# Optimization experiments

Measured on AMD Instinct MI355X. Metric: run time of the kernel, lower is better.

The kernel has to match this reference:

```python
import jax, jax.numpy as jnp
import numpy as np

VOCAB = 50257
NUM_TAGS = 50
EMB_DIM = 128
CTX = 2
N_TOKENS = 262144


def setup_inputs() -> dict:
    key = jax.random.key(0)
    k1, k2, k3, k4 = jax.random.split(key, 4)
    tokens = jax.random.randint(k1, (N_TOKENS,), 0, VOCAB, dtype=jnp.int64 if jax.config.jax_enable_x64 else jnp.int32)
    emb_table = jax.random.normal(k2, (VOCAB, EMB_DIM), dtype=jnp.float32)
    W = jax.random.normal(k3, (NUM_TAGS, EMB_DIM * (1 + 2 * CTX)), dtype=jnp.float32) * 0.05
    b = jax.random.normal(k4, (NUM_TAGS,), dtype=jnp.float32) * 0.05
    return {"tokens": tokens, "emb_table": emb_table, "W": W, "b": b}


def reference(tokens, emb_table, W, b):
    # [N, D] embedding gather
    emb = emb_table[tokens]
    n = emb.shape[0]
    # zero-pad CTX positions on each side (matches torch.zeros_like padding)
    padded = jnp.pad(emb, ((CTX, CTX), (0, 0)))
    # sliding window concat: [N, (2*CTX+1)*D] via 2*CTX+1 shifted views
    windows = jnp.concatenate([padded[i:i + n] for i in range(2 * CTX + 1)], axis=-1)
    logits = windows @ W.T + b  # [N, num_tags]
    log_probs = jax.nn.log_softmax(logits, axis=-1)
    return log_probs
```

## Files before the change

### kernel.cpp

```cpp
#include <hip/hip_runtime.h>
#include <hip/hip_bf16.h>

#define VOCAB 50257
#define NTAGS 50
#define EMB   128
#define NTOK  262144
#define KD    640
#define WPAD  64

#define TAGP  64
#define NZ    320
#define ZROWS 50304

#define TOK   24
#define RWS   28
#define CHR   40
#define NCHUNK (RWS*CHR)
#define NITER  ((NCHUNK+63)/64)

typedef __attribute__((ext_vector_type(4))) float f32x4;
typedef __attribute__((ext_vector_type(8))) short bf16x8;

__device__ __forceinline__ ushort f2bf(float f) {
    union { float f; unsigned u; } v; v.f = f;
    unsigned u = v.u;
    return (ushort)((u + 0x7fffu + ((u >> 16) & 1u)) >> 16);
}

__device__ __forceinline__ void gload_lds16(const void* g, void* l) {
    __builtin_amdgcn_global_load_lds(
        (const __attribute__((address_space(1))) unsigned*)g,
        (__attribute__((address_space(3))) unsigned*)l, 16, 0, 0);
}


__global__ void conv_k(const float* __restrict__ W, ushort* __restrict__ Wt) {
    int g = blockIdx.x * blockDim.x + threadIdx.x;
    if (g >= NZ * 16) return;
    int n = g >> 4, j = g & 15;
    int tg = n & 63, p = n >> 6;
    bf16x8 val = (bf16x8){0,0,0,0,0,0,0,0};
    if (tg < NTAGS) {
        const float* wp = W + tg * KD + p * EMB + j * 8;
        f32x4 lo = *(const f32x4*)wp;
        f32x4 hi = *(const f32x4*)(wp + 4);
        val[0]=(short)f2bf(lo[0]); val[1]=(short)f2bf(lo[1]);
        val[2]=(short)f2bf(lo[2]); val[3]=(short)f2bf(lo[3]);
        val[4]=(short)f2bf(hi[0]); val[5]=(short)f2bf(hi[1]);
        val[6]=(short)f2bf(hi[2]); val[7]=(short)f2bf(hi[3]);
    }
    *(bf16x8*)((char*)Wt + n * 256 + ((j ^ (n & 7)) << 4)) = val;
}

__global__ __launch_bounds__(256)
void zt_k(const float* __restrict__ emb, const ushort* __restrict__ Wt,
          ushort* __restrict__ ZT) {
    __shared__ __align__(16) char wlds[NZ * EMB * 2];

    const int tid  = threadIdx.x;
    const int lane = tid & 63;
    const int wave = tid >> 6;
    const int c = lane & 15, q = lane >> 4;
    const int vb = blockIdx.x * 128;

    f32x4 Elo[2][4], Ehi[2][4];
    #pragma unroll
    for (int nv = 0; nv < 2; ++nv) {
        int row = vb + wave * 32 + nv * 16 + c;
        bool ok = row < VOCAB;
        const float* rp = emb + (size_t)(ok ? row : 0) * EMB;
        #pragma unroll
        for (int kk = 0; kk < 4; ++kk) {
            Elo[nv][kk] = ok ? *(const f32x4*)(rp + kk * 32 + q * 8)
                             : (f32x4){0,0,0,0};
            Ehi[nv][kk] = ok ? *(const f32x4*)(rp + kk * 32 + q * 8 + 4)
                             : (f32x4){0,0,0,0};
        }
    }

    #pragma unroll
    for (int it = 0; it < 20; ++it) {
        int g = it * 256 + tid;
        gload_lds16((const char*)Wt + g * 16, wlds + it * 4096 + (tid >> 6) * 1024 + (tid & 63) * 16);
    }

    bf16x8 E[2][4];
    #pragma unroll
    for (int nv = 0; nv < 2; ++nv)
        #pragma unroll
        for (int kk = 0; kk < 4; ++kk) {
            bf16x8 a;
            a[0]=(short)f2bf(Elo[nv][kk][0]); a[1]=(short)f2bf(Elo[nv][kk][1]);
            a[2]=(short)f2bf(Elo[nv][kk][2]); a[3]=(short)f2bf(Elo[nv][kk][3]);
            a[4]=(short)f2bf(Ehi[nv][kk][0]); a[5]=(short)f2bf(Ehi[nv][kk][1]);
            a[6]=(short)f2bf(Ehi[nv][kk][2]); a[7]=(short)f2bf(Ehi[nv][kk][3]);
            E[nv][kk] = a;
        }
    __syncthreads();

    #pragma unroll
    for (int ng = 0; ng < 5; ++ng) {
        bf16x8 Wf[4][4];
        #pragma unroll
        for (int mtag = 0; mtag < 4; ++mtag) {
            #pragma unroll
            for (int kk = 0; kk < 4; ++kk) {
                int r  = ng * 64 + mtag * 16 + c;
                int ph = (kk * 4 + q) ^ (c & 7);
                Wf[mtag][kk] = *(const bf16x8*)(wlds + r * 256 + ph * 16);
            }
        }
        f32x4 acc[4][2];
        #pragma unroll
        for (int mtag = 0; mtag < 4; ++mtag)
            #pragma unroll
            for (int nv = 0; nv < 2; ++nv)
                acc[mtag][nv] = (f32x4){0.f,0.f,0.f,0.f};
        #pragma unroll
        for (int kk = 0; kk < 4; ++kk)
            #pragma unroll
            for (int mtag = 0; mtag < 4; ++mtag)
                #pragma unroll
                for (int nv = 0; nv < 2; ++nv)
                    acc[mtag][nv] = __builtin_amdgcn_mfma_f32_16x16x32_bf16(
                        Wf[mtag][kk], E[nv][kk], acc[mtag][nv], 0, 0, 0);
        #pragma unroll
        for (int nv = 0; nv < 2; ++nv) {
            const size_t row = (size_t)(vb + wave * 32 + nv * 16 + c);
            #pragma unroll
            for (int mtag = 0; mtag < 4; ++mtag) {
                ushort4 o = { f2bf(acc[mtag][nv][0]), f2bf(acc[mtag][nv][1]),
                              f2bf(acc[mtag][nv][2]), f2bf(acc[mtag][nv][3]) };
                *(ushort4*)(ZT + row * NZ + ng * 64 + mtag * 16 + q * 4) = o;
            }
        }
    }
}

__global__ __launch_bounds__(64, 1)
void tag_k(const int* __restrict__ tokens, const ushort* __restrict__ ZT,
           const float* __restrict__ bias, float* __restrict__ out) {
    __shared__ __align__(16) char smem[RWS * 640 + 128];
    int* ids = (int*)(smem + RWS * 640);

    const int l  = threadIdx.x;
    const int bb = blockIdx.x * TOK;

    {
        int t = bb - 2 + l;
        if (l < RWS) ids[l] = ((unsigned)t < NTOK) ? tokens[t] : VOCAB;
    }
    __syncthreads();

    int tk[NITER];
    #pragma unroll
    for (int w = 0; w < NITER; ++w) {
        int g = w * 64 + l;
        int r = (g < NCHUNK) ? (g / CHR) : 0;
        tk[w] = ids[r];
    }

    #pragma unroll
    for (int w = 0; w < NITER; ++w) {
        int g = w * 64 + l;
        if (g < NCHUNK) {
            int r  = g / CHR;
            int ch = g - r * CHR;
            int i  = ch & 7, p = ch >> 3;
            const char* src = (const char*)ZT + (size_t)tk[w] * 640
                              + p * 128 + ((i ^ (r & 7)) << 4);
            gload_lds16(src, smem + w * 1024);
        }
    }
    __syncthreads();

    float acc[56];
    #pragma unroll
    for (int g = 0; g < 12; ++g) {
        float4 b4 = *(const float4*)(bias + g * 4);
        acc[g*4+0] = b4.x; acc[g*4+1] = b4.y; acc[g*4+2] = b4.z; acc[g*4+3] = b4.w;
    }
    acc[48] = bias[48]; acc[49] = bias[49];
    #pragma unroll
    for (int j = 50; j < 56; ++j) acc[j] = 0.f;

    {
        const int le = (l < TOK) ? l : (TOK - 1);
        bf16x8 v[5][7];
        #pragma unroll
        for (int p = 0; p < 5; ++p) {
            const int rp = le + p;
            const char* rb = smem + rp * 640;
            const int rx = (rp & 7) << 4;
            #pragma unroll
            for (int j = 0; j < 7; ++j)
                v[p][j] = *(const bf16x8*)(rb + p * 128 + ((j << 4) ^ rx));
        }
        #pragma unroll
        for (int p = 0; p < 5; ++p)
            #pragma unroll
            for (int j = 0; j < 7; ++j)
                #pragma unroll
                for (int e = 0; e < 8; ++e) {
                    unsigned u = (unsigned)(ushort)v[p][j][e] << 16;
                    acc[j*8+e] += __uint_as_float(u);
                }
    }

    float m = acc[0];
    #pragma unroll
    for (int j = 1; j < NTAGS; ++j) m = fmaxf(m, acc[j]);
    float s = 0.f;
    #pragma unroll
    for (int j = 0; j < NTAGS; ++j) s += __expf(acc[j] - m);
    const float L = m + __logf(s);

    __syncthreads();
    if (l < TOK) {
        #pragma unroll
        for (int k = 0; k < 25; ++k) {
            float2 st = { acc[2*k] - L, acc[2*k+1] - L };
            *(float2*)(smem + (size_t)l * 200 + k * 8) = st;
        }
    }
    __syncthreads();
    const int nvalid = (NTOK - bb < TOK) ? (NTOK - bb) : TOK;
    const int nbytes = nvalid * 200;
    char* ob = (char*)out + (size_t)bb * 200;
    #pragma unroll
    for (int w = 0; w < 5; ++w) {
        int off = w * 1024 + l * 16;
        if (off < nbytes) {
            f32x4 d = *(const f32x4*)(smem + off);
            __builtin_nontemporal_store(d, (f32x4*)(ob + off));
        }
    }
}

__global__ void fb_conv_k(const float* __restrict__ emb, const float* __restrict__ W,
                          ushort* __restrict__ embb, ushort* __restrict__ wb) {
    const int etotal = (VOCAB + 1) * EMB;
    int idx = (blockIdx.x * blockDim.x + threadIdx.x) * 4;
    if (idx < etotal) {
        float4 v = {0.f, 0.f, 0.f, 0.f};
        if (idx < VOCAB * EMB) v = *(const float4*)(emb + idx);
        ushort4 o = { f2bf(v.x), f2bf(v.y), f2bf(v.z), f2bf(v.w) };
        *(ushort4*)(embb + idx) = o;
    } else {
        int wi = idx - etotal;
        if (wi < WPAD * KD) {
            #pragma unroll
            for (int k = 0; k < 4; ++k) {
                int j = wi + k;
                int tag = j / KD;
                wb[j] = f2bf(tag < NTAGS ? W[j] : 0.f);
            }
        }
    }
}

__global__ __launch_bounds__(64, 2)
void fb_tag_k(const int* __restrict__ tokens, const ushort* __restrict__ embb,
              const ushort* __restrict__ Wb, const float* __restrict__ bias,
              float* __restrict__ out) {
    __shared__ ushort smem[68 * EMB];
    const int lane = threadIdx.x & 63;
    const int c = lane & 15;
    const int q = lane >> 4;
    const int bb = blockIdx.x * 64;
    const int rsub = lane >> 4;

    int tokid[17];
    #pragma unroll
    for (int g = 0; g < 17; ++g) {
        int t = bb - 2 + g * 4 + rsub;
        tokid[g] = (t >= 0 && t < NTOK) ? tokens[t] : VOCAB;
    }
    const ushort* bp[4];
    #pragma unroll
    for (int nt = 0; nt < 4; ++nt)
        bp[nt] = Wb + (nt * 16 + c) * KD + q * 8;
    bf16x8 Bb[4][4];
    #pragma unroll
    for (int s = 0; s < 4; ++s)
        #pragma unroll
        for (int nt = 0; nt < 4; ++nt)
            Bb[s][nt] = *(const bf16x8*)(bp[nt] + (s >> 2) * 128 + (s & 3) * 32);
    float bv[4];
    #pragma unroll
    for (int nt = 0; nt < 4; ++nt) {
        int tag = nt * 16 + c;
        bv[nt] = bias[tag < NTAGS ? tag : NTAGS - 1];
    }
    {
        const int pc = lane & 15;
        #pragma unroll
        for (int g = 0; g < 17; ++g) {
            int i = g * 4 + rsub;
            int sc = pc ^ (i & 7);
            gload_lds16(embb + (size_t)tokid[g] * EMB + sc * 8, (char*)smem + g * 1024);
        }
    }
    __syncthreads();

    f32x4 acc[4][4];
    #pragma unroll
    for (int mt = 0; mt < 4; ++mt)
        #pragma unroll
        for (int nt = 0; nt < 4; ++nt)
            acc[mt][nt] = (f32x4){0.f, 0.f, 0.f, 0.f};
    bf16x8 Ab[2][4];
    #pragma unroll
    for (int s = 0; s < 2; ++s) {
        int p = s >> 2, kk = s & 3;
        int ch = (4 * kk + q) ^ ((c + p) & 7);
        const char* ab = (const char*)smem + (c + p) * 256 + ch * 16;
        #pragma unroll
        for (int mt = 0; mt < 4; ++mt)
            Ab[s][mt] = *(const bf16x8*)(ab + mt * 4096);
    }
    #pragma unroll
    for (int s = 0; s < 20; ++s) {
        __builtin_amdgcn_s_setprio(1);
        #pragma unroll
        for (int mt = 0; mt < 4; ++mt)
            #pragma unroll
            for (int nt = 0; nt < 4; ++nt)
                acc[mt][nt] = __builtin_amdgcn_mfma_f32_16x16x32_bf16(
                    Ab[s & 1][mt], Bb[s & 3][nt], acc[mt][nt], 0, 0, 0);
        __builtin_amdgcn_s_setprio(0);
        if (s + 4 < 20) {
            const int tt = s + 4, p = tt >> 2, kk = tt & 3;
            #pragma unroll
            for (int nt = 0; nt < 4; ++nt)
                Bb[s & 3][nt] = *(const bf16x8*)(bp[nt] + p * 128 + kk * 32);
        }
        if (s + 2 < 20) {
            const int tt = s + 2, p = tt >> 2, kk = tt & 3;
            int ch = (4 * kk + q) ^ ((c + p) & 7);
            const char* ab = (const char*)smem + (c + p) * 256 + ch * 16;
            #pragma unroll
            for (int mt = 0; mt < 4; ++mt)
                Ab[s & 1][mt] = *(const bf16x8*)(ab + mt * 4096);
        }
    }
    #pragma unroll
    for (int mt = 0; mt < 4; ++mt) {
        #pragma unroll
        for (int j = 0; j < 4; ++j) {
            const int row = bb + mt * 16 + q * 4 + j;
            float x[4];
            float m = -1e30f;
            #pragma unroll
            for (int nt = 0; nt < 4; ++nt) {
                float xv = acc[mt][nt][j] + bv[nt];
                x[nt] = xv;
                if (nt * 16 + c < NTAGS) m = fmaxf(m, xv);
            }
            #pragma unroll
            for (int mask = 8; mask >= 1; mask >>= 1)
                m = fmaxf(m, __shfl_xor(m, mask));
            float s = 0.f;
            #pragma unroll
            for (int nt = 0; nt < 4; ++nt)
                if (nt * 16 + c < NTAGS) s += __expf(x[nt] - m);
            #pragma unroll
            for (int mask = 8; mask >= 1; mask >>= 1)
                s += __shfl_xor(s, mask);
            const float L = m + __logf(s);
            #pragma unroll
            for (int nt = 0; nt < 4; ++nt) {
                int tag = nt * 16 + c;
                if (tag < NTAGS) out[row * NTAGS + tag] = x[nt] - L;
            }
        }
    }
}

extern "C" void kernel_launch(void* const* d_in, const int* in_sizes, int n_in,
                              void* d_out, int out_size, void* d_ws, size_t ws_size,
                              hipStream_t stream) {
    const int*   tokens = (const int*)d_in[0];
    const float* emb    = (const float*)d_in[1];
    const float* W      = (const float*)d_in[2];
    const float* b      = (const float*)d_in[3];
    float* out = (float*)d_out;

    const size_t NEED = 81920ull + (size_t)ZROWS * NZ * 2ull;
    if (ws_size >= NEED) {
        ushort* Wt = (ushort*)d_ws;
        ushort* ZT = (ushort*)((char*)d_ws + 81920);
        conv_k<<<20, 256, 0, stream>>>(W, Wt);
        zt_k<<<ZROWS / 128, 256, 0, stream>>>(emb, Wt, ZT);
        tag_k<<<(NTOK + TOK - 1) / TOK, 64, 0, stream>>>(tokens, ZT, b, out);
    } else {
        ushort* embb = (ushort*)d_ws;
        ushort* Wb   = embb + (size_t)(VOCAB + 1) * EMB;
        const int etotal = (VOCAB + 1) * EMB;
        const int total4 = (etotal + WPAD * KD) / 4;
        fb_conv_k<<<(total4 + 255) / 256, 256, 0, stream>>>(emb, W, embb, Wb);
        fb_tag_k<<<NTOK / 64, 64, 0, stream>>>(tokens, embb, Wb, b, out);
    }
}
```

Before: 68.72 us.

## Process two token tiles per tag block with overlapped gather and compute

```diff
diff --git a/kernel.cpp b/kernel.cpp
--- a/kernel.cpp
+++ b/kernel.cpp
@@ -17,6 +17,7 @@
 #define CHR   40
 #define NCHUNK (RWS*CHR)
 #define NITER  ((NCHUNK+63)/64)
+#define TILEB  17920
 
 typedef __attribute__((ext_vector_type(4))) float f32x4;
 typedef __attribute__((ext_vector_type(8))) short bf16x8;
@@ -59,9 +60,9 @@
 
     const int tid  = threadIdx.x;
     const int lane = tid & 63;
-    const int wave = tid >> 6;
     const int c = lane & 15, q = lane >> 4;
     const int vb = blockIdx.x * 128;
+    const int wave = tid >> 6;
 
     f32x4 Elo[2][4], Ehi[2][4];
     #pragma unroll
@@ -81,7 +82,7 @@
     #pragma unroll
     for (int it = 0; it < 20; ++it) {
         int g = it * 256 + tid;
-        gload_lds16((const char*)Wt + g * 16, wlds + it * 4096 + (tid >> 6) * 1024 + (tid & 63) * 16);
+        gload_lds16((const char*)Wt + g * 16, wlds + it * 4096 + wave * 1024);
     }
 
     bf16x8 E[2][4];
@@ -140,24 +141,25 @@
 __global__ __launch_bounds__(64, 1)
 void tag_k(const int* __restrict__ tokens, const ushort* __restrict__ ZT,
            const float* __restrict__ bias, float* __restrict__ out) {
-    __shared__ __align__(16) char smem[RWS * 640 + 128];
-    int* ids = (int*)(smem + RWS * 640);
+    __shared__ __align__(16) char smem[2 * TILEB + 224];
+    int* ids = (int*)(smem + 2 * TILEB);
 
     const int l  = threadIdx.x;
-    const int bb = blockIdx.x * TOK;
-
-    {
-        int t = bb - 2 + l;
-        if (l < RWS) ids[l] = ((unsigned)t < NTOK) ? tokens[t] : VOCAB;
+    const long bb = (long)blockIdx.x * 48;
+
+    if (l < 52) {
+        long t = bb - 2 + l;
+        ids[l] = (t >= 0 && t < NTOK) ? tokens[t] : VOCAB;
     }
     __syncthreads();
 
-    int tk[NITER];
+    int tkA[NITER], tkB[NITER];
     #pragma unroll
     for (int w = 0; w < NITER; ++w) {
         int g = w * 64 + l;
         int r = (g < NCHUNK) ? (g / CHR) : 0;
-        tk[w] = ids[r];
+        tkA[w] = ids[r];
+        tkB[w] = ids[24 + r];
     }
 
     #pragma unroll
@@ -167,68 +169,124 @@
             int r  = g / CHR;
             int ch = g - r * CHR;
             int i  = ch & 7, p = ch >> 3;
-            const char* src = (const char*)ZT + (size_t)tk[w] * 640
-                              + p * 128 + ((i ^ (r & 7)) << 4);
-            gload_lds16(src, smem + w * 1024);
-        }
-    }
-    __syncthreads();
-
-    float acc[56];
-    #pragma unroll
-    for (int g = 0; g < 12; ++g) {
-        float4 b4 = *(const float4*)(bias + g * 4);
-        acc[g*4+0] = b4.x; acc[g*4+1] = b4.y; acc[g*4+2] = b4.z; acc[g*4+3] = b4.w;
-    }
-    acc[48] = bias[48]; acc[49] = bias[49];
-    #pragma unroll
-    for (int j = 50; j < 56; ++j) acc[j] = 0.f;
-
+            gload_lds16((const char*)ZT + (size_t)tkA[w] * 640
+                        + p * 128 + ((i ^ (r & 7)) << 4), smem + w * 1024);
+        }
+    }
+    #pragma unroll
+    for (int w = 0; w < NITER; ++w) {
+        int g = w * 64 + l;
+        if (g < NCHUNK) {
+            int r  = g / CHR;
+            int ch = g - r * CHR;
+            int i  = ch & 7, p = ch >> 3;
+            gload_lds16((const char*)ZT + (size_t)tkB[w] * 640
+                        + p * 128 + ((i ^ (r & 7)) << 4), smem + TILEB + w * 1024);
+        }
+    }
+
+    float b48 = bias[48], b49 = bias[49];
+    float4 bv[12];
+    #pragma unroll
+    for (int g = 0; g < 12; ++g) bv[g] = *(const float4*)(bias + g * 4);
+
+    asm volatile("s_waitcnt vmcnt(18)" ::: "memory");
+    __builtin_amdgcn_sched_barrier(0);
     {
+        float acc[56];
+        #pragma unroll
+        for (int g = 0; g < 12; ++g) {
+            acc[g*4+0] = bv[g].x; acc[g*4+1] = bv[g].y;
+            acc[g*4+2] = bv[g].z; acc[g*4+3] = bv[g].w;
+        }
+        acc[48] = b48; acc[49] = b49;
+        #pragma unroll
+        for (int j = 50; j < 56; ++j) acc[j] = 0.f;
+
         const int le = (l < TOK) ? l : (TOK - 1);
-        bf16x8 v[5][7];
         #pragma unroll
         for (int p = 0; p < 5; ++p) {
             const int rp = le + p;
             const char* rb = smem + rp * 640;
             const int rx = (rp & 7) << 4;
             #pragma unroll
-            for (int j = 0; j < 7; ++j)
-                v[p][j] = *(const bf16x8*)(rb + p * 128 + ((j << 4) ^ rx));
-        }
-        #pragma unroll
-        for (int p = 0; p < 5; ++p)
-            #pragma unroll
-            for (int j = 0; j < 7; ++j)
+            for (int j = 0; j < 7; ++j) {
+                bf16x8 v = *(const bf16x8*)(rb + p * 128 + ((j << 4) ^ rx));
                 #pragma unroll
                 for (int e = 0; e < 8; ++e) {
-                    unsigned u = (unsigned)(ushort)v[p][j][e] << 16;
+                    unsigned u = (unsigned)(ushort)v[e] << 16;
                     acc[j*8+e] += __uint_as_float(u);
                 }
-    }
-
-    float m = acc[0];
-    #pragma unroll
-    for (int j = 1; j < NTAGS; ++j) m = fmaxf(m, acc[j]);
-    float s = 0.f;
-    #pragma unroll
-    for (int j = 0; j < NTAGS; ++j) s += __expf(acc[j] - m);
-    const float L = m + __logf(s);
-
-    __syncthreads();
-    if (l < TOK) {
-        #pragma unroll
-        for (int k = 0; k < 25; ++k) {
-            float2 st = { acc[2*k] - L, acc[2*k+1] - L };
-            *(float2*)(smem + (size_t)l * 200 + k * 8) = st;
-        }
-    }
-    __syncthreads();
-    const int nvalid = (NTOK - bb < TOK) ? (NTOK - bb) : TOK;
-    const int nbytes = nvalid * 200;
+            }
+        }
+        float m = acc[0];
+        #pragma unroll
+        for (int j = 1; j < NTAGS; ++j) m = fmaxf(m, acc[j]);
+        float s = 0.f;
+        #pragma unroll
+        for (int j = 0; j < NTAGS; ++j) s += __expf(acc[j] - m);
+        const float L = m + __logf(s);
+        if (l < TOK) {
+            #pragma unroll
+            for (int k = 0; k < 25; ++k) {
+                float2 st = { acc[2*k] - L, acc[2*k+1] - L };
+                *(float2*)(smem + (size_t)l * 200 + k * 8) = st;
+            }
+        }
+    }
+
+    asm volatile("s_waitcnt vmcnt(0)" ::: "memory");
+    __builtin_amdgcn_sched_barrier(0);
+    {
+        float acc[56];
+        #pragma unroll
+        for (int g = 0; g < 12; ++g) {
+            acc[g*4+0] = bv[g].x; acc[g*4+1] = bv[g].y;
+            acc[g*4+2] = bv[g].z; acc[g*4+3] = bv[g].w;
+        }
+        acc[48] = b48; acc[49] = b49;
+        #pragma unroll
+        for (int j = 50; j < 56; ++j) acc[j] = 0.f;
+
+        const int le = (l < TOK) ? l : (TOK - 1);
+        #pragma unroll
+        for (int p = 0; p < 5; ++p) {
+            const int rp = le + p;
+            const char* rb = smem + TILEB + rp * 640;
+            const int rx = (rp & 7) << 4;
+            #pragma unroll
+            for (int j = 0; j < 7; ++j) {
+                bf16x8 v = *(const bf16x8*)(rb + p * 128 + ((j << 4) ^ rx));
+                #pragma unroll
+                for (int e = 0; e < 8; ++e) {
+                    unsigned u = (unsigned)(ushort)v[e] << 16;
+                    acc[j*8+e] += __uint_as_float(u);
+                }
+            }
+        }
+        float m = acc[0];
+        #pragma unroll
+        for (int j = 1; j < NTAGS; ++j) m = fmaxf(m, acc[j]);
+        float s = 0.f;
+        #pragma unroll
+        for (int j = 0; j < NTAGS; ++j) s += __expf(acc[j] - m);
+        const float L = m + __logf(s);
+        if (l < TOK) {
+            #pragma unroll
+            for (int k = 0; k < 25; ++k) {
+                float2 st = { acc[2*k] - L, acc[2*k+1] - L };
+                *(float2*)(smem + (size_t)(24 + l) * 200 + k * 8) = st;
+            }
+        }
+    }
+
+    asm volatile("s_waitcnt lgkmcnt(0)" ::: "memory");
+    __builtin_amdgcn_sched_barrier(0);
+    const long nvalid = (NTOK - bb < 48) ? (NTOK - bb) : 48;
+    const int nbytes = (int)(nvalid * 200);
     char* ob = (char*)out + (size_t)bb * 200;
     #pragma unroll
-    for (int w = 0; w < 5; ++w) {
+    for (int w = 0; w < 10; ++w) {
         int off = w * 1024 + l * 16;
         if (off < nbytes) {
             f32x4 d = *(const f32x4*)(smem + off);
@@ -392,7 +450,8 @@
         ushort* ZT = (ushort*)((char*)d_ws + 81920);
         conv_k<<<20, 256, 0, stream>>>(W, Wt);
         zt_k<<<ZROWS / 128, 256, 0, stream>>>(emb, Wt, ZT);
-        tag_k<<<(NTOK + TOK - 1) / TOK, 64, 0, stream>>>(tokens, ZT, b, out);
+        const int nblk = (int)((NTOK + 47) / 48);
+        tag_k<<<nblk, 64, 0, stream>>>(tokens, ZT, b, out);
     } else {
         ushort* embb = (ushort*)d_ws;
         ushort* Wb   = embb + (size_t)(VOCAB + 1) * EMB;
```

New measurement: 76.14 us. 10.8% more time.
